# Kernel tuning notes

Measured on AMD Instinct MI355X. Metric: run time of the kernel, lower is better.

## Reference

```python
import jax, jax.numpy as jnp
import numpy as np

K = 1  # top-k from init_kwargs


def setup_inputs() -> dict:
    key = jax.random.key(0)
    k0, k1, k2, k3, k4, k5 = jax.random.split(key, 6)
    B, L, Ed, NE = 8192, 1024, 1024, 8
    D = L + Ed  # input_dim = latent_dim + embed_dim
    s = 1.0 / np.sqrt(D)  # torch nn.Linear default init bound
    x = jax.random.normal(k0, (B, L), dtype=jnp.float32)
    y = jax.random.normal(k1, (B, Ed), dtype=jnp.float32)
    We = jax.random.uniform(k2, (NE, D, D), dtype=jnp.float32, minval=-s, maxval=s)  # expert weights [E, out, in]
    be = jax.random.uniform(k3, (NE, D), dtype=jnp.float32, minval=-s, maxval=s)
    gW = jax.random.uniform(k4, (NE, D), dtype=jnp.float32, minval=-s, maxval=s)  # gate weight [E, in]
    gb = jax.random.uniform(k5, (NE,), dtype=jnp.float32, minval=-s, maxval=s)
    return {"x": x, "y": y, "We": We, "be": be, "gW": gW, "gb": gb}


def reference(x, y, We, be, gW, gb):
    # inp: [B, D]
    inp = jnp.concatenate([x, y], axis=1)
    # gate logits: [B, E] (eval mode: no noise)
    gate_logits = inp @ gW.T + gb
    topk_val, topk_idx = jax.lax.top_k(gate_logits, K)  # [B, K]
    topk_gates = jax.nn.softmax(topk_val, axis=1)       # [B, K]
    # dense compute-all-experts (faithful to original): [B, E, D]
    all_out = jnp.einsum('bd,eod->beo', inp, We) + be[None, :, :]
    # gather top-k experts per token: [B, K, D]
    gathered = jnp.take_along_axis(all_out, topk_idx[:, :, None], axis=1)
    fused = jnp.sum(gathered * topk_gates[:, :, None], axis=1)  # [B, D]
    return fused
```

## Files before the change

### kernel.cpp

```cpp
#include <hip/hip_runtime.h>
#include <stdint.h>

#define B_TOK 8192
#define DIM   2048
#define NE    8
#define BM 128
#define BN 128
#define BK 64
#define CVT_BLOCKS 8192
#define GATE_BLOCKS 2048
#define NT3 32

typedef __bf16 bf16x8 __attribute__((ext_vector_type(8)));
typedef float  f32x4  __attribute__((ext_vector_type(4)));

__device__ __forceinline__ unsigned short f2b(float f) {
  unsigned u = __builtin_bit_cast(unsigned, f);
  u += 0x7fffu + ((u >> 16) & 1u);
  return (unsigned short)(u >> 16);
}
__device__ __forceinline__ uint2 pack4(float4 v) {
  uint2 r;
  r.x = (unsigned)f2b(v.x) | ((unsigned)f2b(v.y) << 16);
  r.y = (unsigned)f2b(v.z) | ((unsigned)f2b(v.w) << 16);
  return r;
}
__device__ __forceinline__ void gload16(const void* g, void* l) {
  __builtin_amdgcn_global_load_lds(
      (const __attribute__((address_space(1))) void*)g,
      (__attribute__((address_space(3))) void*)l, 16, 0, 0);
}

template <bool FULL>
__global__ __launch_bounds__(256) void gate_cvt(
    const float* __restrict__ x,
    const float* __restrict__ y,
    const float* __restrict__ gW,
    const float* __restrict__ gb,
    const float* __restrict__ We,
    int* __restrict__ eid,
    unsigned short* __restrict__ inpB,
    unsigned short* __restrict__ WeB) {
  const int bid = blockIdx.x;
  if (FULL && bid >= GATE_BLOCKS) {
    const int cb = bid - GATE_BLOCKS;
    const size_t base = (size_t)cb * 1024;
#pragma unroll
    for (int j = 0; j < 4; ++j) {
      size_t i4 = base + (size_t)(j * 256 + threadIdx.x);
      float4 v = *(const float4*)(We + i4 * 4);
      *(uint2*)(WeB + i4 * 4) = pack4(v);
    }
    return;
  }

  const int tid = threadIdx.x;
  const int ln = tid & 63;
  const int token = bid * 4 + (tid >> 6);

  double acc[NE];
#pragma unroll
  for (int e = 0; e < NE; ++e) acc[e] = 0.0;

  const float* bases[2] = {x, y};
#pragma unroll
  for (int p = 0; p < 2; ++p) {
    const float* rowp = bases[p] + (size_t)token * 1024;
#pragma unroll
    for (int it = 0; it < 4; ++it) {
      const int d = it * 256 + ln * 4;
      float4 v = *(const float4*)(rowp + d);
      if (FULL)
        *(uint2*)(inpB + (size_t)token * DIM + p * 1024 + d) = pack4(v);
#pragma unroll
      for (int e = 0; e < NE; ++e) {
        float4 g = *(const float4*)(gW + e * DIM + p * 1024 + d);
        acc[e] += (double)v.x * (double)g.x + (double)v.y * (double)g.y +
                  (double)v.z * (double)g.z + (double)v.w * (double)g.w;
      }
    }
  }
#pragma unroll
  for (int e = 0; e < NE; ++e) {
#pragma unroll
    for (int off = 32; off >= 1; off >>= 1) acc[e] += __shfl_xor(acc[e], off, 64);
  }
  if (ln == 0) {
    int best = 0;
    double bv = acc[0] + (double)gb[0];
#pragma unroll
    for (int e = 1; e < NE; ++e) {
      double v = acc[e] + (double)gb[e];
      if (v > bv) { bv = v; best = e; }
    }
    eid[token] = best;
  }
}

__global__ __launch_bounds__(256) void bucket8(const int* __restrict__ eid,
                                               int* __restrict__ counts,
                                               int* __restrict__ perm) {
  const int e = blockIdx.x;
  const int tid = threadIdx.x, ln = tid & 63, wv = tid >> 6;
  __shared__ int wsum[4];
  __shared__ int basev;
  if (tid == 0) basev = 0;
  __syncthreads();
  for (int t0 = 0; t0 < B_TOK; t0 += 256) {
    int t = t0 + tid;
    bool m = (eid[t] == e);
    unsigned long long mk = __ballot(m);
    int pre = __popcll(mk & ((1ull << ln) - 1ull));
    if (ln == 0) wsum[wv] = __popcll(mk);
    __syncthreads();
    int off = basev;
    for (int w = 0; w < wv; ++w) off += wsum[w];
    if (m) perm[e * B_TOK + off + pre] = t;
    __syncthreads();
    if (tid == 0) basev += wsum[0] + wsum[1] + wsum[2] + wsum[3];
    __syncthreads();
  }
  if (tid == 0) counts[e] = basev;
}

__global__ __launch_bounds__(512, 2) void moe_gemm3(
    const float* __restrict__ be,
    const unsigned short* __restrict__ inpB,
    const unsigned short* __restrict__ WeB,
    const int* __restrict__ counts,
    const int* __restrict__ perm,
    float* __restrict__ out) {
  __shared__ __align__(16) unsigned short AB[65536];
  __shared__ int tokLds[256];

  const int e = blockIdx.z;
  const int cnt = counts[e];
  const int m0 = blockIdx.y * 256;
  if (m0 >= cnt) return;
  const int n0 = blockIdx.x * 256;

  const int tid = threadIdx.x;
  const int ln = tid & 63;
  const int wv = tid >> 6;
  const int wm = wv & 1;
  const int wn = wv >> 1;

  if (tid < 256) {
    int r = m0 + tid;
    tokLds[tid] = perm[e * B_TOK + (r < cnt ? r : cnt - 1)];
  }
  __syncthreads();

  const int g = (ln & 7) ^ (ln >> 3);
  const unsigned short* wbbase = WeB + (size_t)e * DIM * DIM;
  const unsigned short* aS[2][2];
  const unsigned short* bS[2][2];
#pragma unroll
  for (int h = 0; h < 2; ++h)
#pragma unroll
    for (int i = 0; i < 2; ++i) {
      int row = h * 128 + (wv * 2 + i) * 8 + (ln >> 3);
      aS[h][i] = inpB + (size_t)tokLds[row] * DIM + g * 8;
      bS[h][i] = wbbase + (size_t)(n0 + row) * DIM + g * 8;
    }

  f32x4 acc[8][4];
#pragma unroll
  for (int a = 0; a < 8; ++a)
#pragma unroll
    for (int b = 0; b < 4; ++b) acc[a][b] = (f32x4){0.f, 0.f, 0.f, 0.f};

  auto STG = [&](int kt, int h) {
    const int d = (kt & 1) * 16384;
    const int ko = kt * 64;
    gload16(aS[h][0] + ko, &AB[d + h * 8192 + (wv * 2 + 0) * 512]);
    gload16(aS[h][1] + ko, &AB[d + h * 8192 + (wv * 2 + 1) * 512]);
    gload16(bS[h][0] + ko, &AB[32768 + d + h * 8192 + (wv * 2 + 0) * 512]);
    gload16(bS[h][1] + ko, &AB[32768 + d + h * 8192 + (wv * 2 + 1) * 512]);
  };

  auto PHASE = [&](int kt, int mh, int nh) {
    const int d = (kt & 1) * 16384;
    bf16x8 av[4][2], bv[2][2];
#pragma unroll
    for (int f = 0; f < 4; ++f)
#pragma unroll
      for (int ks = 0; ks < 2; ++ks) {
        int r = wm * 128 + mh * 64 + f * 16 + (ln & 15);
        int c = ks * 4 + (ln >> 4);
        av[f][ks] = *(const bf16x8*)&AB[d + r * 64 + ((c ^ (ln & 7))) * 8];
      }
#pragma unroll
    for (int j = 0; j < 2; ++j)
#pragma unroll
      for (int ks = 0; ks < 2; ++ks) {
        int r = wn * 64 + nh * 32 + j * 16 + (ln & 15);
        int c = ks * 4 + (ln >> 4);
        bv[j][ks] = *(const bf16x8*)&AB[32768 + d + r * 64 + ((c ^ (ln & 7))) * 8];
      }
    __builtin_amdgcn_s_setprio(1);
#pragma unroll
    for (int f = 0; f < 4; ++f)
#pragma unroll
      for (int j = 0; j < 2; ++j)
#pragma unroll
        for (int ks = 0; ks < 2; ++ks)
          acc[mh * 4 + f][nh * 2 + j] = __builtin_amdgcn_mfma_f32_16x16x32_bf16(
              av[f][ks], bv[j][ks], acc[mh * 4 + f][nh * 2 + j], 0, 0, 0);
    __builtin_amdgcn_s_setprio(0);
  };

  STG(0, 0); STG(0, 1);

  for (int kt = 0; kt < NT3; ++kt) {
    if (kt + 1 < NT3) {
      STG(kt + 1, 0);
      asm volatile("s_waitcnt vmcnt(4)" ::: "memory");
    } else {
      asm volatile("s_waitcnt vmcnt(0)" ::: "memory");
    }
    __builtin_amdgcn_s_barrier();
    PHASE(kt, 0, 0);
    __builtin_amdgcn_s_barrier();
    if (kt + 1 < NT3) STG(kt + 1, 1);
    PHASE(kt, 0, 1);
    __builtin_amdgcn_s_barrier();
    PHASE(kt, 1, 1);
    __builtin_amdgcn_s_barrier();
    PHASE(kt, 1, 0);
    __builtin_amdgcn_s_barrier();
  }

  float bias[4]; int col[4];
#pragma unroll
  for (int b = 0; b < 4; ++b) {
    col[b] = n0 + wn * 64 + b * 16 + (ln & 15);
    bias[b] = be[e * DIM + col[b]];
  }
#pragma unroll
  for (int a = 0; a < 8; ++a) {
    int rbase = wm * 128 + a * 16 + ((ln >> 4) << 2);
#pragma unroll
    for (int r = 0; r < 4; ++r) {
      int rl = rbase + r;
      if (m0 + rl < cnt) {
        size_t t = (size_t)tokLds[rl];
#pragma unroll
        for (int b = 0; b < 4; ++b)
          out[t * DIM + col[b]] = acc[a][b][r] + bias[b];
      }
    }
  }
}

__global__ __launch_bounds__(256) void moe_gemm_f32(
    const float* __restrict__ x,
    const float* __restrict__ y,
    const float* __restrict__ We,
    const float* __restrict__ be,
    const int* __restrict__ counts,
    const int* __restrict__ perm,
    float* __restrict__ out) {
  __shared__ unsigned short As[BM * BK];
  __shared__ unsigned short Bs[BN * BK];
  __shared__ int tokLds[BM];

  const int e = blockIdx.z;
  const int cnt = counts[e];
  const int m0 = blockIdx.y * BM;
  if (m0 >= cnt) return;
  const int n0 = blockIdx.x * BN;

  const int tid = threadIdx.x;
  const int ln = tid & 63;
  const int wv = tid >> 6;
  const int wm = wv & 1, wn = wv >> 1;

  if (tid < BM) {
    int r = m0 + tid;
    tokLds[tid] = perm[e * B_TOK + (r < cnt ? r : cnt - 1)];
  }
  __syncthreads();

  const float* wfbase = We + (size_t)e * DIM * DIM;

  f32x4 acc[4][4];
#pragma unroll
  for (int i = 0; i < 4; ++i)
#pragma unroll
    for (int j = 0; j < 4; ++j) acc[i][j] = (f32x4){0.f, 0.f, 0.f, 0.f};

  for (int k0 = 0; k0 < DIM; k0 += BK) {
    __syncthreads();
    const float* ab = (k0 < 1024) ? x : y;
    const int kk = k0 & 1023;
#pragma unroll
    for (int i = 0; i < 8; ++i) {
      int li = i * 256 + tid;
      int row = li >> 4, k4 = li & 15;
      int chunk = k4 >> 1, half = k4 & 1;
      int slot = (chunk ^ (row & 7)) * 2 + half;
      int tok = tokLds[row];
      float4 va = *(const float4*)(ab + (size_t)tok * 1024 + kk + k4 * 4);
      *(uint2*)&As[row * BK + slot * 4] = pack4(va);
      float4 vb = *(const float4*)(wfbase + (size_t)(n0 + row) * DIM + k0 + k4 * 4);
      *(uint2*)&Bs[row * BK + slot * 4] = pack4(vb);
    }
    __syncthreads();

#pragma unroll
    for (int ks = 0; ks < 2; ++ks) {
      bf16x8 av[4], bv[4];
#pragma unroll
      for (int i = 0; i < 4; ++i) {
        int rA = wm * 64 + i * 16 + (ln & 15);
        int c = ks * 4 + (ln >> 4);
        av[i] = *(const bf16x8*)&As[rA * BK + (c ^ (rA & 7)) * 8];
      }
#pragma unroll
      for (int j = 0; j < 4; ++j) {
        int rB = wn * 64 + j * 16 + (ln & 15);
        int c = ks * 4 + (ln >> 4);
        bv[j] = *(const bf16x8*)&Bs[rB * BK + (c ^ (rB & 7)) * 8];
      }
#pragma unroll
      for (int i = 0; i < 4; ++i)
#pragma unroll
        for (int j = 0; j < 4; ++j)
          acc[i][j] = __builtin_amdgcn_mfma_f32_16x16x32_bf16(av[i], bv[j], acc[i][j], 0, 0, 0);
    }
  }

  float bias[4]; int col[4];
#pragma unroll
  for (int j = 0; j < 4; ++j) {
    col[j] = n0 + wn * 64 + j * 16 + (ln & 15);
    bias[j] = be[e * DIM + col[j]];
  }
#pragma unroll
  for (int i = 0; i < 4; ++i) {
    int rbase = wm * 64 + i * 16 + ((ln >> 4) << 2);
#pragma unroll
    for (int r = 0; r < 4; ++r) {
      int rl = rbase + r;
      if (m0 + rl < cnt) {
        size_t t = (size_t)tokLds[rl];
#pragma unroll
        for (int j = 0; j < 4; ++j)
          out[t * DIM + col[j]] = acc[i][j][r] + bias[j];
      }
    }
  }
}

extern "C" void kernel_launch(void* const* d_in, const int* in_sizes, int n_in,
                              void* d_out, int out_size, void* d_ws, size_t ws_size,
                              hipStream_t stream) {
  const float* x  = (const float*)d_in[0];
  const float* y  = (const float*)d_in[1];
  const float* We = (const float*)d_in[2];
  const float* be = (const float*)d_in[3];
  const float* gW = (const float*)d_in[4];
  const float* gb = (const float*)d_in[5];
  float* out = (float*)d_out;

  char* ws = (char*)d_ws;
  int* counts = (int*)ws;
  int* eid    = (int*)(ws + 256);
  int* perm   = (int*)(ws + 33024);
  unsigned short* inpB = (unsigned short*)(ws + 295168);
  unsigned short* WeB  = (unsigned short*)(ws + 33849600);
  const size_t needed = 33849600ull + 67108864ull;

  if (ws_size >= needed) {
    gate_cvt<true><<<dim3(GATE_BLOCKS + CVT_BLOCKS), 256, 0, stream>>>(
        x, y, gW, gb, We, eid, inpB, WeB);
    bucket8<<<dim3(NE), 256, 0, stream>>>(eid, counts, perm);
    moe_gemm3<<<dim3(DIM / 256, B_TOK / 256, NE), 512, 0, stream>>>(
        be, inpB, WeB, counts, perm, out);
  } else {
    gate_cvt<false><<<dim3(GATE_BLOCKS), 256, 0, stream>>>(
        x, y, gW, gb, nullptr, eid, nullptr, nullptr);
    bucket8<<<dim3(NE), 256, 0, stream>>>(eid, counts, perm);
    moe_gemm_f32<<<dim3(DIM / BN, B_TOK / BM, NE), 256, 0, stream>>>(
        x, y, We, be, counts, perm, out);
  }
}
```

Measured before the change: 482.3 us.

## Restage GEMM pipeline with early B prefetch and move weight conversion into bucket launch

The main GEMM loop is rescheduled. B tiles are now prefetched two k-steps ahead and A tiles one step ahead, and LDS fragment reads are interleaved with MFMA quadrants behind sched_barrier-fenced barriers, so global loads and LDS reads overlap compute better. The fp32-to-bf16 weight conversion moves from the gate kernel into the bucket kernel's launch, so the serial 8-block bucketing runs alongside the bulk conversion instead of after it. The deeper prefetch puts more loads in flight and adds barriers, and the 64KB LDS buffer layout has to hold the two-step-ahead B tiles without overwriting data still being read.

Result: faster. 429.4 us (-11.0%).

```diff
diff --git a/kernel.cpp b/kernel.cpp
--- a/kernel.cpp
+++ b/kernel.cpp
@@ -8,7 +8,6 @@
 #define BN 128
 #define BK 64
 #define CVT_BLOCKS 8192
-#define GATE_BLOCKS 2048
 #define NT3 32
 
 typedef __bf16 bf16x8 __attribute__((ext_vector_type(8)));
@@ -31,32 +30,20 @@
       (__attribute__((address_space(3))) void*)l, 16, 0, 0);
 }
 
-template <bool FULL>
-__global__ __launch_bounds__(256) void gate_cvt(
+#define SCHEDB __builtin_amdgcn_sched_barrier(0)
+#define BARRIER do { SCHEDB; __builtin_amdgcn_s_barrier(); SCHEDB; } while (0)
+
+template <bool WINP>
+__global__ __launch_bounds__(256) void gate_kernel(
     const float* __restrict__ x,
     const float* __restrict__ y,
     const float* __restrict__ gW,
     const float* __restrict__ gb,
-    const float* __restrict__ We,
     int* __restrict__ eid,
-    unsigned short* __restrict__ inpB,
-    unsigned short* __restrict__ WeB) {
-  const int bid = blockIdx.x;
-  if (FULL && bid >= GATE_BLOCKS) {
-    const int cb = bid - GATE_BLOCKS;
-    const size_t base = (size_t)cb * 1024;
-#pragma unroll
-    for (int j = 0; j < 4; ++j) {
-      size_t i4 = base + (size_t)(j * 256 + threadIdx.x);
-      float4 v = *(const float4*)(We + i4 * 4);
-      *(uint2*)(WeB + i4 * 4) = pack4(v);
-    }
-    return;
-  }
-
+    unsigned short* __restrict__ inpB) {
   const int tid = threadIdx.x;
   const int ln = tid & 63;
-  const int token = bid * 4 + (tid >> 6);
+  const int token = blockIdx.x * 4 + (tid >> 6);
 
   double acc[NE];
 #pragma unroll
@@ -70,7 +57,7 @@
     for (int it = 0; it < 4; ++it) {
       const int d = it * 256 + ln * 4;
       float4 v = *(const float4*)(rowp + d);
-      if (FULL)
+      if (WINP)
         *(uint2*)(inpB + (size_t)token * DIM + p * 1024 + d) = pack4(v);
 #pragma unroll
       for (int e = 0; e < NE; ++e) {
@@ -97,9 +84,25 @@
   }
 }
 
-__global__ __launch_bounds__(256) void bucket8(const int* __restrict__ eid,
-                                               int* __restrict__ counts,
-                                               int* __restrict__ perm) {
+template <bool CVT>
+__global__ __launch_bounds__(256) void bucket_cvt(
+    const int* __restrict__ eid,
+    int* __restrict__ counts,
+    int* __restrict__ perm,
+    const float* __restrict__ We,
+    unsigned short* __restrict__ WeB) {
+  if (CVT && blockIdx.x >= NE) {
+    const int cb = blockIdx.x - NE;
+    const size_t base = (size_t)cb * 1024;
+#pragma unroll
+    for (int j = 0; j < 4; ++j) {
+      size_t i4 = base + (size_t)(j * 256 + threadIdx.x);
+      float4 v = *(const float4*)(We + i4 * 4);
+      *(uint2*)(WeB + i4 * 4) = pack4(v);
+    }
+    return;
+  }
+
   const int e = blockIdx.x;
   const int tid = threadIdx.x, ln = tid & 63, wv = tid >> 6;
   __shared__ int wsum[4];
@@ -123,7 +126,7 @@
   if (tid == 0) counts[e] = basev;
 }
 
-__global__ __launch_bounds__(512, 2) void moe_gemm3(
+__global__ __launch_bounds__(512, 2) void moe_gemm4(
     const float* __restrict__ be,
     const unsigned short* __restrict__ inpB,
     const unsigned short* __restrict__ WeB,
@@ -170,65 +173,83 @@
 #pragma unroll
     for (int b = 0; b < 4; ++b) acc[a][b] = (f32x4){0.f, 0.f, 0.f, 0.f};
 
-  auto STG = [&](int kt, int h) {
-    const int d = (kt & 1) * 16384;
-    const int ko = kt * 64;
-    gload16(aS[h][0] + ko, &AB[d + h * 8192 + (wv * 2 + 0) * 512]);
-    gload16(aS[h][1] + ko, &AB[d + h * 8192 + (wv * 2 + 1) * 512]);
-    gload16(bS[h][0] + ko, &AB[32768 + d + h * 8192 + (wv * 2 + 0) * 512]);
-    gload16(bS[h][1] + ko, &AB[32768 + d + h * 8192 + (wv * 2 + 1) * 512]);
+  const int aBase = (wm * 128 + (ln & 15)) * 64;
+  const int bBase = (wn * 64 + (ln & 15)) * 64;
+  const int ofk0 = (((ln >> 4)) ^ (ln & 7)) * 8;
+  const int ofk1 = ((4 + (ln >> 4)) ^ (ln & 7)) * 8;
+
+  auto SA = [&](int tt, int h) {
+    if (tt >= NT3) return;
+    const int dd = (tt & 1) * 16384;
+    const int ko = tt * 64;
+    gload16(aS[h][0] + ko, &AB[dd + h * 8192 + (wv * 2 + 0) * 512]);
+    gload16(aS[h][1] + ko, &AB[dd + h * 8192 + (wv * 2 + 1) * 512]);
   };
-
-  auto PHASE = [&](int kt, int mh, int nh) {
-    const int d = (kt & 1) * 16384;
-    bf16x8 av[4][2], bv[2][2];
+  auto SBst = [&](int tt, int h) {
+    if (tt >= NT3) return;
+    const int dd = (tt & 1) * 16384;
+    const int ko = tt * 64;
+    gload16(bS[h][0] + ko, &AB[32768 + dd + h * 8192 + (wv * 2 + 0) * 512]);
+    gload16(bS[h][1] + ko, &AB[32768 + dd + h * 8192 + (wv * 2 + 1) * 512]);
+  };
+  auto RAV = [&](bf16x8 (&av)[4][2], int d, int mq) {
+#pragma unroll
+    for (int f = 0; f < 4; ++f) {
+      av[f][0] = *(const bf16x8*)&AB[d + aBase + mq * 4096 + f * 1024 + ofk0];
+      av[f][1] = *(const bf16x8*)&AB[d + aBase + mq * 4096 + f * 1024 + ofk1];
+    }
+  };
+  auto RBV = [&](bf16x8 (&bv)[2][2], int d, int nq) {
+#pragma unroll
+    for (int j = 0; j < 2; ++j) {
+      bv[j][0] = *(const bf16x8*)&AB[32768 + d + bBase + nq * 2048 + j * 1024 + ofk0];
+      bv[j][1] = *(const bf16x8*)&AB[32768 + d + bBase + nq * 2048 + j * 1024 + ofk1];
+    }
+  };
+  auto QM = [&](int mq, int nq, bf16x8 (&av)[4][2], bf16x8 (&bv)[2][2]) {
+    __builtin_amdgcn_s_setprio(1);
 #pragma unroll
     for (int f = 0; f < 4; ++f)
 #pragma unroll
-      for (int ks = 0; ks < 2; ++ks) {
-        int r = wm * 128 + mh * 64 + f * 16 + (ln & 15);
-        int c = ks * 4 + (ln >> 4);
-        av[f][ks] = *(const bf16x8*)&AB[d + r * 64 + ((c ^ (ln & 7))) * 8];
-      }
-#pragma unroll
-    for (int j = 0; j < 2; ++j)
-#pragma unroll
-      for (int ks = 0; ks < 2; ++ks) {
-        int r = wn * 64 + nh * 32 + j * 16 + (ln & 15);
-        int c = ks * 4 + (ln >> 4);
-        bv[j][ks] = *(const bf16x8*)&AB[32768 + d + r * 64 + ((c ^ (ln & 7))) * 8];
-      }
-    __builtin_amdgcn_s_setprio(1);
-#pragma unroll
-    for (int f = 0; f < 4; ++f)
-#pragma unroll
       for (int j = 0; j < 2; ++j)
 #pragma unroll
         for (int ks = 0; ks < 2; ++ks)
-          acc[mh * 4 + f][nh * 2 + j] = __builtin_amdgcn_mfma_f32_16x16x32_bf16(
-              av[f][ks], bv[j][ks], acc[mh * 4 + f][nh * 2 + j], 0, 0, 0);
+          acc[mq * 4 + f][nq * 2 + j] = __builtin_amdgcn_mfma_f32_16x16x32_bf16(
+              av[f][ks], bv[j][ks], acc[mq * 4 + f][nq * 2 + j], 0, 0, 0);
     __builtin_amdgcn_s_setprio(0);
   };
 
-  STG(0, 0); STG(0, 1);
-
-  for (int kt = 0; kt < NT3; ++kt) {
-    if (kt + 1 < NT3) {
-      STG(kt + 1, 0);
+  SA(0, 0); SA(0, 1); SBst(0, 0); SBst(0, 1); SBst(1, 0); SBst(1, 1);
+  asm volatile("s_waitcnt vmcnt(4)" ::: "memory");
+  BARRIER;
+
+  for (int t = 0; t < NT3; ++t) {
+    const int d = (t & 1) * 16384;
+    bf16x8 av[4][2], bv0[2][2], bv1[2][2];
+    RAV(av, d, 0); RBV(bv0, d, 0);
+    SA(t + 1, 0);
+    BARRIER;
+    QM(0, 0, av, bv0);
+    BARRIER;
+    RBV(bv1, d, 1);
+    SA(t + 1, 1);
+    BARRIER;
+    QM(0, 1, av, bv1);
+    BARRIER;
+    RAV(av, d, 1);
+    SBst(t + 2, 0);
+    BARRIER;
+    QM(1, 1, av, bv1);
+    BARRIER;
+    SBst(t + 2, 1);
+    if (t < NT3 - 2) {
       asm volatile("s_waitcnt vmcnt(4)" ::: "memory");
     } else {
       asm volatile("s_waitcnt vmcnt(0)" ::: "memory");
     }
-    __builtin_amdgcn_s_barrier();
-    PHASE(kt, 0, 0);
-    __builtin_amdgcn_s_barrier();
-    if (kt + 1 < NT3) STG(kt + 1, 1);
-    PHASE(kt, 0, 1);
-    __builtin_amdgcn_s_barrier();
-    PHASE(kt, 1, 1);
-    __builtin_amdgcn_s_barrier();
-    PHASE(kt, 1, 0);
-    __builtin_amdgcn_s_barrier();
+    BARRIER;
+    QM(1, 0, av, bv0);
+    BARRIER;
   }
 
   float bias[4]; int col[4];
@@ -373,15 +394,13 @@
   const size_t needed = 33849600ull + 67108864ull;
 
   if (ws_size >= needed) {
-    gate_cvt<true><<<dim3(GATE_BLOCKS + CVT_BLOCKS), 256, 0, stream>>>(
-        x, y, gW, gb, We, eid, inpB, WeB);
-    bucket8<<<dim3(NE), 256, 0, stream>>>(eid, counts, perm);
-    moe_gemm3<<<dim3(DIM / 256, B_TOK / 256, NE), 512, 0, stream>>>(
+    gate_kernel<true><<<dim3(B_TOK / 4), 256, 0, stream>>>(x, y, gW, gb, eid, inpB);
+    bucket_cvt<true><<<dim3(NE + CVT_BLOCKS), 256, 0, stream>>>(eid, counts, perm, We, WeB);
+    moe_gemm4<<<dim3(DIM / 256, B_TOK / 256, NE), 512, 0, stream>>>(
         be, inpB, WeB, counts, perm, out);
   } else {
-    gate_cvt<false><<<dim3(GATE_BLOCKS), 256, 0, stream>>>(
-        x, y, gW, gb, nullptr, eid, nullptr, nullptr);
-    bucket8<<<dim3(NE), 256, 0, stream>>>(eid, counts, perm);
+    gate_kernel<false><<<dim3(B_TOK / 4), 256, 0, stream>>>(x, y, gW, gb, eid, nullptr);
+    bucket_cvt<false><<<dim3(NE), 256, 0, stream>>>(eid, counts, perm, nullptr, nullptr);
     moe_gemm_f32<<<dim3(DIM / BN, B_TOK / BM, NE), 256, 0, stream>>>(
         x, y, We, be, counts, perm, out);
   }
```
